# Kernel optimization log

Hardware: AMD Instinct MI355X
Metric: run time of the kernel (lower is better)

Reference implementation:

```python
import jax, jax.numpy as jnp
import numpy as np
from jax import lax


def setup_inputs() -> dict:
    key = jax.random.key(0)
    k1, k2, k3, k4 = jax.random.split(key, 4)
    H = 2048
    L = 3
    hidden_states = jax.random.normal(k1, (2, 4096, H), dtype=jnp.float32)
    Win = jax.random.normal(k2, (3 * H, H), dtype=jnp.float32) * (H ** -0.5)
    conv_w = jax.random.normal(k3, (H, 1, L), dtype=jnp.float32) * (L ** -0.5)
    Wout = jax.random.normal(k4, (H, H), dtype=jnp.float32) * (H ** -0.5)
    return {"hidden_states": hidden_states, "Win": Win, "conv_w": conv_w, "Wout": Wout}


def reference(hidden_states, Win, conv_w, Wout):
    H = hidden_states.shape[-1]
    L = conv_w.shape[-1]
    BCx = jnp.einsum('bsh,oh->bso', hidden_states, Win)  # (b, s, 3H)
    B, C, x = jnp.split(BCx, 3, axis=-1)
    Bx = jnp.transpose(B * x, (0, 2, 1))  # (b, H, s)
    # depthwise causal conv: left-pad L-1 so output length == s (torch pads both
    # sides then slices [..., :seqlen]; left-only padding is equivalent)
    conv_out = lax.conv_general_dilated(
        Bx, conv_w, window_strides=(1,), padding=[(L - 1, 0)],
        feature_group_count=H, dimension_numbers=('NCH', 'OIH', 'NCH'))
    y = C * jnp.transpose(conv_out, (0, 2, 1))  # (b, s, H)
    return jnp.einsum('bsh,oh->bso', y, Wout)
```

## Files before the change

### kernel.cpp

```cpp
#include <hip/hip_runtime.h>
#include <hip/hip_bf16.h>

typedef unsigned short u16;
typedef __attribute__((ext_vector_type(8))) short bf16x8;
typedef __attribute__((ext_vector_type(16))) float f32x16;

static __device__ __forceinline__ u16 f2bf(float f) {
    unsigned u = __float_as_uint(f);
    unsigned r = (u + 0x7fffu + ((u >> 16) & 1u)) >> 16;
    return (u16)r;
}
static __device__ __forceinline__ float bf2f(u16 u) {
    return __uint_as_float(((unsigned)u) << 16);
}

static __device__ __forceinline__ void async_copy16(const void* gptr, void* lptr) {
    __builtin_amdgcn_global_load_lds(
        (const __attribute__((address_space(1))) void*)gptr,
        (__attribute__((address_space(3))) void*)lptr, 16, 0, 0);
}

__global__ __launch_bounds__(256)
void cvt_all(const float* __restrict__ a, const float* __restrict__ b,
             const float* __restrict__ c,
             u16* __restrict__ oa, u16* __restrict__ ob, u16* __restrict__ oc) {
    int blk = blockIdx.x;
    const float* src; u16* dst; long base;
    if (blk < 16384)      { src = a; dst = oa; base = blk; }
    else if (blk < 28672) { src = b; dst = ob; base = blk - 16384; }
    else                  { src = c; dst = oc; base = blk - 28672; }
    long i = (base * 256 + threadIdx.x) * 4;
    float4 f = *(const float4*)(src + i);
    u16 o[4] = { f2bf(f.x), f2bf(f.y), f2bf(f.z), f2bf(f.w) };
    *(uint2*)(dst + i) = *(const uint2*)o;
}

template<bool BF16_OUT>
__global__ __launch_bounds__(256, 2)
void gemm_bt(const u16* __restrict__ A, const u16* __restrict__ B,
             void* __restrict__ Cout, int M, int N, int K) {
    __shared__ __align__(16) u16 As[256 * 32];
    __shared__ __align__(16) u16 Bs[128 * 32];

    const int t    = threadIdx.x;
    const int wave = t >> 6;
    const int lane = t & 63;
    const int wm   = (wave >> 1) * 128;
    const int wn   = (wave & 1) * 64;
    const int half = lane >> 5;
    const int l32  = lane & 31;

    const int id   = blockIdx.y * gridDim.x + blockIdx.x;
    const int cpx  = gridDim.x >> 3;
    const int xcd  = id & 7;
    const int loc  = id >> 3;
    const int bx   = xcd * cpx + (loc % cpx);
    const int by   = loc / cpx;

    const int rowA = by * 256;
    const int rowB = bx * 128;

    const int ar = t >> 2;
    const int ac = ((t & 3) ^ ((ar >> 1) & 3)) * 8;
    const u16* Ag[4]; const u16* Bg[2];
#pragma unroll
    for (int i = 0; i < 4; i++) Ag[i] = A + (long)(rowA + i * 64 + ar) * K + ac;
#pragma unroll
    for (int i = 0; i < 2; i++) Bg[i] = B + (long)(rowB + i * 64 + ar) * K + ac;
    u16* Asl[4]; u16* Bsl[2];
#pragma unroll
    for (int i = 0; i < 4; i++) Asl[i] = As + i * 2048 + t * 8;
#pragma unroll
    for (int i = 0; i < 2; i++) Bsl[i] = Bs + i * 2048 + t * 8;

    f32x16 acc[4][2] = {};

    for (int k0 = 0; k0 < K; k0 += 32) {
        __syncthreads();
#pragma unroll
        for (int i = 0; i < 4; i++) async_copy16(Ag[i] + k0, Asl[i]);
#pragma unroll
        for (int i = 0; i < 2; i++) async_copy16(Bg[i] + k0, Bsl[i]);
        __syncthreads();

        bf16x8 af[4][2], bg[2][2];
#pragma unroll
        for (int mi = 0; mi < 4; mi++)
#pragma unroll
            for (int ks = 0; ks < 2; ks++) {
                int row = wm + mi * 32 + l32;
                af[mi][ks] = *(const bf16x8*)(
                    As + row * 32 + (((ks * 2 + half) ^ ((row >> 1) & 3)) * 8));
            }
#pragma unroll
        for (int nj = 0; nj < 2; nj++)
#pragma unroll
            for (int ks = 0; ks < 2; ks++) {
                int row = wn + nj * 32 + l32;
                bg[nj][ks] = *(const bf16x8*)(
                    Bs + row * 32 + (((ks * 2 + half) ^ ((row >> 1) & 3)) * 8));
            }
#pragma unroll
        for (int ks = 0; ks < 2; ks++)
#pragma unroll
            for (int mi = 0; mi < 4; mi++)
#pragma unroll
                for (int nj = 0; nj < 2; nj++)
                    acc[mi][nj] = __builtin_amdgcn_mfma_f32_32x32x16_bf16(
                        af[mi][ks], bg[nj][ks], acc[mi][nj], 0, 0, 0);
    }

#pragma unroll
    for (int mi = 0; mi < 4; mi++) {
#pragma unroll
        for (int nj = 0; nj < 2; nj++) {
#pragma unroll
            for (int r = 0; r < 16; r++) {
                int rowt = (r & 3) + 8 * (r >> 2) + 4 * half;
                long m = rowA + wm + mi * 32 + rowt;
                long n = rowB + wn + nj * 32 + l32;
                float v = acc[mi][nj][r];
                if (BF16_OUT) ((u16*)Cout)[m * N + n] = f2bf(v);
                else          ((float*)Cout)[m * N + n] = v;
            }
        }
    }
}

union U16x8 { uint4 v; u16 u[8]; };

__global__ __launch_bounds__(256)
void conv_fuse(const u16* __restrict__ BCx, const float* __restrict__ cw,
               u16* __restrict__ y) {
    const int row = blockIdx.x;
    const int h0  = threadIdx.x * 8;
    const int sl  = row & 4095;
    const u16* r0 = BCx + (long)row * 6144;

    U16x8 B0, X0, C0, B1, X1, B2, X2;
    B0.v = *(const uint4*)(r0 + h0);
    C0.v = *(const uint4*)(r0 + 2048 + h0);
    X0.v = *(const uint4*)(r0 + 4096 + h0);
    if (sl >= 1) {
        B1.v = *(const uint4*)(r0 - 6144 + h0);
        X1.v = *(const uint4*)(r0 - 6144 + 4096 + h0);
    } else { B1.v = make_uint4(0,0,0,0); X1.v = make_uint4(0,0,0,0); }
    if (sl >= 2) {
        B2.v = *(const uint4*)(r0 - 12288 + h0);
        X2.v = *(const uint4*)(r0 - 12288 + 4096 + h0);
    } else { B2.v = make_uint4(0,0,0,0); X2.v = make_uint4(0,0,0,0); }

    U16x8 o;
#pragma unroll
    for (int i = 0; i < 8; i++) {
        int h = h0 + i;
        float bx0 = bf2f(B0.u[i]) * bf2f(X0.u[i]);
        float bx1 = bf2f(B1.u[i]) * bf2f(X1.u[i]);
        float bx2 = bf2f(B2.u[i]) * bf2f(X2.u[i]);
        float v = cw[h*3+2] * bx0 + cw[h*3+1] * bx1 + cw[h*3] * bx2;
        o.u[i] = f2bf(v * bf2f(C0.u[i]));
    }
    *(uint4*)(y + (long)row * 2048 + h0) = o.v;
}

extern "C" void kernel_launch(void* const* d_in, const int* in_sizes, int n_in,
                              void* d_out, int out_size, void* d_ws, size_t ws_size,
                              hipStream_t stream) {
    const float* hs   = (const float*)d_in[0];
    const float* Win  = (const float*)d_in[1];
    const float* cw   = (const float*)d_in[2];
    const float* Wout = (const float*)d_in[3];
    float* out = (float*)d_out;

    char* ws = (char*)d_ws;
    u16* hsb   = (u16*)(ws);
    u16* Winb  = (u16*)(ws +  33554432);
    u16* Woutb = (u16*)(ws +  58720256);
    u16* bcx   = (u16*)(ws +  67108864);
    u16* yb    = (u16*)(ws + 167772160);

    cvt_all<<<32768, 256, 0, stream>>>(hs, Win, Wout, hsb, Winb, Woutb);

    gemm_bt<true ><<<dim3(48, 32), 256, 0, stream>>>(hsb, Winb, bcx, 8192, 6144, 2048);

    conv_fuse<<<8192, 256, 0, stream>>>(bcx, cw, yb);

    gemm_bt<false><<<dim3(16, 32), 256, 0, stream>>>(yb, Woutb, out, 8192, 2048, 2048);
}
```

Measured before the change: 504.5 us.

## Rewrite bf16 GEMM as 8-wave 256x256 tile with double-buffered LDS pipeline

Result: faster. 437.0 us (-13.4%).

```diff
diff --git a/kernel.cpp b/kernel.cpp
--- a/kernel.cpp
+++ b/kernel.cpp
@@ -3,7 +3,7 @@
 
 typedef unsigned short u16;
 typedef __attribute__((ext_vector_type(8))) short bf16x8;
-typedef __attribute__((ext_vector_type(16))) float f32x16;
+typedef __attribute__((ext_vector_type(4))) float f32x4;
 
 static __device__ __forceinline__ u16 f2bf(float f) {
     unsigned u = __float_as_uint(f);
@@ -36,92 +36,158 @@
 }
 
 template<bool BF16_OUT>
-__global__ __launch_bounds__(256, 2)
-void gemm_bt(const u16* __restrict__ A, const u16* __restrict__ B,
-             void* __restrict__ Cout, int M, int N, int K) {
-    __shared__ __align__(16) u16 As[256 * 32];
-    __shared__ __align__(16) u16 Bs[128 * 32];
+__global__ __launch_bounds__(512, 2)
+void gemm_bt8(const u16* __restrict__ A, const u16* __restrict__ B,
+              void* __restrict__ Cout, int M, int N, int K) {
+    __shared__ __align__(16) u16 lds[65536];
 
     const int t    = threadIdx.x;
-    const int wave = t >> 6;
     const int lane = t & 63;
-    const int wm   = (wave >> 1) * 128;
-    const int wn   = (wave & 1) * 64;
-    const int half = lane >> 5;
-    const int l32  = lane & 31;
+    const int wm   = (t >> 6) >> 2;
+    const int wn   = (t >> 6) & 3;
+    const int l15  = lane & 15;
+    const int hi   = lane >> 4;
+    const int l7   = lane & 7;
 
     const int id   = blockIdx.y * gridDim.x + blockIdx.x;
     const int cpx  = gridDim.x >> 3;
-    const int xcd  = id & 7;
-    const int loc  = id >> 3;
-    const int bx   = xcd * cpx + (loc % cpx);
-    const int by   = loc / cpx;
-
-    const int rowA = by * 256;
-    const int rowB = bx * 128;
-
-    const int ar = t >> 2;
-    const int ac = ((t & 3) ^ ((ar >> 1) & 3)) * 8;
-    const u16* Ag[4]; const u16* Bg[2];
-#pragma unroll
-    for (int i = 0; i < 4; i++) Ag[i] = A + (long)(rowA + i * 64 + ar) * K + ac;
-#pragma unroll
-    for (int i = 0; i < 2; i++) Bg[i] = B + (long)(rowB + i * 64 + ar) * K + ac;
-    u16* Asl[4]; u16* Bsl[2];
-#pragma unroll
-    for (int i = 0; i < 4; i++) Asl[i] = As + i * 2048 + t * 8;
-#pragma unroll
-    for (int i = 0; i < 2; i++) Bsl[i] = Bs + i * 2048 + t * 8;
-
-    f32x16 acc[4][2] = {};
-
-    for (int k0 = 0; k0 < K; k0 += 32) {
-        __syncthreads();
-#pragma unroll
-        for (int i = 0; i < 4; i++) async_copy16(Ag[i] + k0, Asl[i]);
-#pragma unroll
-        for (int i = 0; i < 2; i++) async_copy16(Bg[i] + k0, Bsl[i]);
-        __syncthreads();
-
-        bf16x8 af[4][2], bg[2][2];
-#pragma unroll
-        for (int mi = 0; mi < 4; mi++)
-#pragma unroll
-            for (int ks = 0; ks < 2; ks++) {
-                int row = wm + mi * 32 + l32;
-                af[mi][ks] = *(const bf16x8*)(
-                    As + row * 32 + (((ks * 2 + half) ^ ((row >> 1) & 3)) * 8));
-            }
-#pragma unroll
-        for (int nj = 0; nj < 2; nj++)
-#pragma unroll
-            for (int ks = 0; ks < 2; ks++) {
-                int row = wn + nj * 32 + l32;
-                bg[nj][ks] = *(const bf16x8*)(
-                    Bs + row * 32 + (((ks * 2 + half) ^ ((row >> 1) & 3)) * 8));
-            }
+    const int bx   = (id & 7) * cpx + ((id >> 3) % cpx);
+    const int by   = (id >> 3) / cpx;
+    const long rowA = (long)by * 256;
+    const long rowB = (long)bx * 256;
+
+    const int pl0 = t >> 3;
+    const int slotcol = ((t & 7) ^ (pl0 & 7)) * 8;
+    const u16* Asrc[2][2]; const u16* Bsrc[2][2];
+#pragma unroll
+    for (int h = 0; h < 2; h++) {
+        int gA0 = h * 64 + pl0;
+        int gA1 = 128 + h * 64 + pl0;
+        Asrc[h][0] = A + (rowA + gA0) * K + slotcol;
+        Asrc[h][1] = A + (rowA + gA1) * K + slotcol;
+        int nB0 = (pl0 >> 5) * 64 + h * 32 + (pl0 & 31);
+        int nB1 = ((64 + pl0) >> 5) * 64 + h * 32 + (pl0 & 31);
+        Bsrc[h][0] = B + (rowB + nB0) * K + slotcol;
+        Bsrc[h][1] = B + (rowB + nB1) * K + slotcol;
+    }
+    const int t8 = t * 8;
+
+    auto STAGE = [&](int bufo, bool isB, int h, int kk) {
+        const u16* s0 = (isB ? Bsrc : Asrc)[h][0] + kk;
+        const u16* s1 = (isB ? Bsrc : Asrc)[h][1] + kk;
+        u16* d = lds + bufo + (isB ? 16384 : 0) + h * 8192 + t8;
+        async_copy16(s0, d);
+        async_copy16(s1, d + 4096);
+    };
+
+    const int aBase = wm * 4096 + l15 * 64;
+    const int bBase = 16384 + wn * 2048 + l15 * 64;
+    const int sOff0 = (hi ^ l7) * 8;
+    const int sOff1 = ((4 + hi) ^ l7) * 8;
+
+    bf16x8 af[4][2], bg0[2][2], bg1[2][2];
+    f32x4 acc[8][4] = {};
+
+    auto LOAD_AF = [&](int bufo, int Mq) {
+#pragma unroll
+        for (int m = 0; m < 4; m++) {
+            const u16* p = lds + bufo + Mq * 8192 + aBase + m * 1024;
+            af[m][0] = *(const bf16x8*)(p + sOff0);
+            af[m][1] = *(const bf16x8*)(p + sOff1);
+        }
+    };
+    auto LOAD_BG = [&](int bufo, int Nq, bf16x8 (*bg)[2]) {
+#pragma unroll
+        for (int n = 0; n < 2; n++) {
+            const u16* p = lds + bufo + Nq * 8192 + bBase + n * 1024;
+            bg[n][0] = *(const bf16x8*)(p + sOff0);
+            bg[n][1] = *(const bf16x8*)(p + sOff1);
+        }
+    };
+    auto MFMA_Q = [&](int Mq, int Nq, bf16x8 (*bg)[2]) {
+        __builtin_amdgcn_s_setprio(1);
 #pragma unroll
         for (int ks = 0; ks < 2; ks++)
 #pragma unroll
-            for (int mi = 0; mi < 4; mi++)
-#pragma unroll
-                for (int nj = 0; nj < 2; nj++)
-                    acc[mi][nj] = __builtin_amdgcn_mfma_f32_32x32x16_bf16(
-                        af[mi][ks], bg[nj][ks], acc[mi][nj], 0, 0, 0);
-    }
-
-#pragma unroll
-    for (int mi = 0; mi < 4; mi++) {
-#pragma unroll
-        for (int nj = 0; nj < 2; nj++) {
-#pragma unroll
-            for (int r = 0; r < 16; r++) {
-                int rowt = (r & 3) + 8 * (r >> 2) + 4 * half;
-                long m = rowA + wm + mi * 32 + rowt;
-                long n = rowB + wn + nj * 32 + l32;
+            for (int m = 0; m < 4; m++)
+#pragma unroll
+                for (int n = 0; n < 2; n++)
+                    acc[Mq * 4 + m][Nq * 2 + n] =
+                        __builtin_amdgcn_mfma_f32_16x16x32_bf16(
+                            af[m][ks], bg[n][ks], acc[Mq * 4 + m][Nq * 2 + n],
+                            0, 0, 0);
+        __builtin_amdgcn_s_setprio(0);
+    };
+
+#define BAR()   __builtin_amdgcn_s_barrier()
+#define WAITL() do { asm volatile("s_waitcnt lgkmcnt(0)" ::: "memory"); \
+                     __builtin_amdgcn_sched_barrier(0); } while (0)
+#define VM6()   asm volatile("s_waitcnt vmcnt(6)" ::: "memory")
+
+    STAGE(0, false, 0, 0);  STAGE(0, false, 1, 0);
+    STAGE(0, true,  0, 0);  STAGE(0, true,  1, 0);
+    STAGE(32768, false, 0, 64);
+    STAGE(32768, true,  0, 64);  STAGE(32768, true, 1, 64);
+    VM6();
+    BAR();
+
+#pragma unroll 1
+    for (int k0 = 0; k0 < K; k0 += 128) {
+        int kN1 = k0 + 64;
+        int kN2 = k0 + 128; if (kN2 >= K) kN2 = 0;
+        int kN3 = k0 + 192; if (kN3 >= K) kN3 -= K;
+        LOAD_AF(0, 0); LOAD_BG(0, 0, bg0);
+        STAGE(32768, false, 1, kN1);
+        BAR(); WAITL();
+        MFMA_Q(0, 0, bg0); BAR();
+        LOAD_BG(0, 1, bg1);
+        STAGE(0, false, 0, kN2);
+        BAR(); WAITL();
+        MFMA_Q(0, 1, bg1); BAR();
+        LOAD_AF(0, 1);
+        STAGE(0, true, 0, kN2);
+        BAR(); WAITL();
+        MFMA_Q(1, 0, bg0); BAR();
+        STAGE(0, true, 1, kN2);
+        VM6();
+        BAR();
+        MFMA_Q(1, 1, bg1); BAR();
+        LOAD_AF(32768, 0); LOAD_BG(32768, 0, bg0);
+        STAGE(0, false, 1, kN2);
+        BAR(); WAITL();
+        MFMA_Q(0, 0, bg0); BAR();
+        LOAD_BG(32768, 1, bg1);
+        STAGE(32768, false, 0, kN3);
+        BAR(); WAITL();
+        MFMA_Q(0, 1, bg1); BAR();
+        LOAD_AF(32768, 1);
+        STAGE(32768, true, 0, kN3);
+        BAR(); WAITL();
+        MFMA_Q(1, 0, bg0); BAR();
+        STAGE(32768, true, 1, kN3);
+        VM6();
+        BAR();
+        MFMA_Q(1, 1, bg1); BAR();
+    }
+    asm volatile("s_waitcnt vmcnt(0)" ::: "memory");
+
+#undef BAR
+#undef WAITL
+#undef VM6
+
+    const long crowBase = rowA + wm * 128 + hi * 4;
+    const long ccolBase = rowB + wn * 64 + l15;
+#pragma unroll
+    for (int mi = 0; mi < 8; mi++) {
+#pragma unroll
+        for (int nj = 0; nj < 4; nj++) {
+            long base = (crowBase + mi * 16) * N + ccolBase + nj * 16;
+#pragma unroll
+            for (int r = 0; r < 4; r++) {
                 float v = acc[mi][nj][r];
-                if (BF16_OUT) ((u16*)Cout)[m * N + n] = f2bf(v);
-                else          ((float*)Cout)[m * N + n] = v;
+                long idx = base + (long)r * N;
+                if (BF16_OUT) ((u16*)Cout)[idx] = f2bf(v);
+                else          ((float*)Cout)[idx] = v;
             }
         }
     }
@@ -181,9 +247,9 @@
 
     cvt_all<<<32768, 256, 0, stream>>>(hs, Win, Wout, hsb, Winb, Woutb);
 
-    gemm_bt<true ><<<dim3(48, 32), 256, 0, stream>>>(hsb, Winb, bcx, 8192, 6144, 2048);
+    gemm_bt8<true ><<<dim3(24, 32), 512, 0, stream>>>(hsb, Winb, bcx, 8192, 6144, 2048);
 
     conv_fuse<<<8192, 256, 0, stream>>>(bcx, cw, yb);
 
-    gemm_bt<false><<<dim3(16, 32), 256, 0, stream>>>(yb, Woutb, out, 8192, 2048, 2048);
-}
+    gemm_bt8<false><<<dim3(8, 32), 512, 0, stream>>>(yb, Woutb, out, 8192, 2048, 2048);
+}
```

## Rewrite GEMM as 256x256 tile, 8-wave kernel with 4-stage async LDS pipeline

Applied to the files above, without the earlier changes.

Result: faster. 467.3 us (-7.4%).

```diff
diff --git a/kernel.cpp b/kernel.cpp
--- a/kernel.cpp
+++ b/kernel.cpp
@@ -36,79 +36,94 @@
 }
 
 template<bool BF16_OUT>
-__global__ __launch_bounds__(256, 2)
-void gemm_bt(const u16* __restrict__ A, const u16* __restrict__ B,
-             void* __restrict__ Cout, int M, int N, int K) {
-    __shared__ __align__(16) u16 As[256 * 32];
-    __shared__ __align__(16) u16 Bs[128 * 32];
+__global__ __launch_bounds__(512, 2)
+void gemm_bt8(const u16* __restrict__ A, const u16* __restrict__ B,
+              void* __restrict__ Cout, int M, int N, int K) {
+    __shared__ __align__(16) u16 lds[65536];
 
     const int t    = threadIdx.x;
-    const int wave = t >> 6;
     const int lane = t & 63;
-    const int wm   = (wave >> 1) * 128;
-    const int wn   = (wave & 1) * 64;
-    const int half = lane >> 5;
+    const int wm   = (t >> 6) >> 2;
+    const int wn   = (t >> 6) & 3;
     const int l32  = lane & 31;
+    const int hi   = lane >> 5;
 
     const int id   = blockIdx.y * gridDim.x + blockIdx.x;
     const int cpx  = gridDim.x >> 3;
-    const int xcd  = id & 7;
-    const int loc  = id >> 3;
-    const int bx   = xcd * cpx + (loc % cpx);
-    const int by   = loc / cpx;
-
-    const int rowA = by * 256;
-    const int rowB = bx * 128;
-
-    const int ar = t >> 2;
-    const int ac = ((t & 3) ^ ((ar >> 1) & 3)) * 8;
-    const u16* Ag[4]; const u16* Bg[2];
-#pragma unroll
-    for (int i = 0; i < 4; i++) Ag[i] = A + (long)(rowA + i * 64 + ar) * K + ac;
-#pragma unroll
-    for (int i = 0; i < 2; i++) Bg[i] = B + (long)(rowB + i * 64 + ar) * K + ac;
-    u16* Asl[4]; u16* Bsl[2];
-#pragma unroll
-    for (int i = 0; i < 4; i++) Asl[i] = As + i * 2048 + t * 8;
-#pragma unroll
-    for (int i = 0; i < 2; i++) Bsl[i] = Bs + i * 2048 + t * 8;
-
+    const int bx   = (id & 7) * cpx + ((id >> 3) % cpx);
+    const int by   = (id >> 3) / cpx;
+    const long rowA = (long)by * 256;
+    const long rowB = (long)bx * 256;
+
+    const int sr  = t >> 2;
+    const int kcs = ((t & 3) ^ ((sr >> 1) & 3)) * 8;
+    const u16* Asrc0 = A + (rowA + sr) * (long)K + kcs;
+    const u16* Asrc1 = Asrc0 + 128 * (long)K;
+    const u16* Bsrc0 = B + (rowB + sr) * (long)K + kcs;
+    const u16* Bsrc1 = Bsrc0 + 128 * (long)K;
+    u16* const dA = lds + t * 8;
+    u16* const dB = lds + 8192 + t * 8;
+
+    const int sw = (l32 >> 1) & 3;
+    const int c0 = (hi ^ sw) * 8;
+    const int c1 = ((2 + hi) ^ sw) * 8;
+    const int aO = (wm * 128 + l32) * 32;
+    const int bO = 8192 + (wn * 64 + l32) * 32;
+
+    bf16x8 afA[4], bgA[2], afB[4], bgB[2];
     f32x16 acc[4][2] = {};
 
-    for (int k0 = 0; k0 < K; k0 += 32) {
-        __syncthreads();
-#pragma unroll
-        for (int i = 0; i < 4; i++) async_copy16(Ag[i] + k0, Asl[i]);
-#pragma unroll
-        for (int i = 0; i < 2; i++) async_copy16(Bg[i] + k0, Bsl[i]);
-        __syncthreads();
-
-        bf16x8 af[4][2], bg[2][2];
-#pragma unroll
-        for (int mi = 0; mi < 4; mi++)
-#pragma unroll
-            for (int ks = 0; ks < 2; ks++) {
-                int row = wm + mi * 32 + l32;
-                af[mi][ks] = *(const bf16x8*)(
-                    As + row * 32 + (((ks * 2 + half) ^ ((row >> 1) & 3)) * 8));
-            }
-#pragma unroll
-        for (int nj = 0; nj < 2; nj++)
-#pragma unroll
-            for (int ks = 0; ks < 2; ks++) {
-                int row = wn + nj * 32 + l32;
-                bg[nj][ks] = *(const bf16x8*)(
-                    Bs + row * 32 + (((ks * 2 + half) ^ ((row >> 1) & 3)) * 8));
-            }
-#pragma unroll
-        for (int ks = 0; ks < 2; ks++)
-#pragma unroll
-            for (int mi = 0; mi < 4; mi++)
-#pragma unroll
-                for (int nj = 0; nj < 2; nj++)
-                    acc[mi][nj] = __builtin_amdgcn_mfma_f32_32x32x16_bf16(
-                        af[mi][ks], bg[nj][ks], acc[mi][nj], 0, 0, 0);
+    auto STAGE_A = [&](int bufo, int kk) {
+        async_copy16(Asrc0 + kk, dA + bufo);
+        async_copy16(Asrc1 + kk, dA + bufo + 4096);
+    };
+    auto STAGE_B = [&](int bufo, int kk) {
+        async_copy16(Bsrc0 + kk, dB + bufo);
+        async_copy16(Bsrc1 + kk, dB + bufo + 4096);
+    };
+    auto LOADS = [&](int bufo, int cOff, bf16x8* af, bf16x8* bg) {
+#pragma unroll
+        for (int m = 0; m < 4; m++)
+            af[m] = *(const bf16x8*)(lds + bufo + aO + m * 1024 + cOff);
+#pragma unroll
+        for (int n = 0; n < 2; n++)
+            bg[n] = *(const bf16x8*)(lds + bufo + bO + n * 1024 + cOff);
+    };
+    auto MF = [&](bf16x8* af, bf16x8* bg) {
+        __builtin_amdgcn_s_setprio(1);
+#pragma unroll
+        for (int m = 0; m < 4; m++)
+#pragma unroll
+            for (int n = 0; n < 2; n++)
+                acc[m][n] = __builtin_amdgcn_mfma_f32_32x32x16_bf16(
+                    af[m], bg[n], acc[m][n], 0, 0, 0);
+        __builtin_amdgcn_s_setprio(0);
+    };
+
+    STAGE_A(0, 0);          STAGE_B(0, 0);
+    STAGE_A(16384, 32);     STAGE_B(16384, 32);
+    STAGE_A(32768, 64);     STAGE_B(32768, 64);
+    asm volatile("s_waitcnt vmcnt(4)" ::: "memory");
+    __builtin_amdgcn_s_barrier();
+    LOADS(0, c0, afA, bgA);
+
+    const int NT = K >> 5;
+#pragma unroll 4
+    for (int i = 0; i < NT; i++) {
+        const int bufR = (i & 3) << 14;
+        const int bufN = ((i + 1) & 3) << 14;
+        const int bufS = ((i + 3) & 3) << 14;
+        int kk = (i + 3) << 5; if (kk >= K) kk = 0;
+        LOADS(bufR, c1, afB, bgB);
+        STAGE_A(bufS, kk);
+        MF(afA, bgA);
+        LOADS(bufN, c0, afA, bgA);
+        STAGE_B(bufS, kk);
+        MF(afB, bgB);
+        asm volatile("s_waitcnt vmcnt(4)" ::: "memory");
+        __builtin_amdgcn_s_barrier();
     }
+    asm volatile("s_waitcnt vmcnt(0)" ::: "memory");
 
 #pragma unroll
     for (int mi = 0; mi < 4; mi++) {
@@ -116,9 +131,9 @@
         for (int nj = 0; nj < 2; nj++) {
 #pragma unroll
             for (int r = 0; r < 16; r++) {
-                int rowt = (r & 3) + 8 * (r >> 2) + 4 * half;
-                long m = rowA + wm + mi * 32 + rowt;
-                long n = rowB + wn + nj * 32 + l32;
+                int rowt = (r & 3) + 8 * (r >> 2) + 4 * hi;
+                long m = rowA + wm * 128 + mi * 32 + rowt;
+                long n = rowB + wn * 64 + nj * 32 + l32;
                 float v = acc[mi][nj][r];
                 if (BF16_OUT) ((u16*)Cout)[m * N + n] = f2bf(v);
                 else          ((float*)Cout)[m * N + n] = v;
@@ -181,9 +196,9 @@
 
     cvt_all<<<32768, 256, 0, stream>>>(hs, Win, Wout, hsb, Winb, Woutb);
 
-    gemm_bt<true ><<<dim3(48, 32), 256, 0, stream>>>(hsb, Winb, bcx, 8192, 6144, 2048);
+    gemm_bt8<true ><<<dim3(24, 32), 512, 0, stream>>>(hsb, Winb, bcx, 8192, 6144, 2048);
 
     conv_fuse<<<8192, 256, 0, stream>>>(bcx, cw, yb);
 
-    gemm_bt<false><<<dim3(16, 32), 256, 0, stream>>>(yb, Woutb, out, 8192, 2048, 2048);
-}
+    gemm_bt8<false><<<dim3(8, 32), 512, 0, stream>>>(yb, Woutb, out, 8192, 2048, 2048);
+}
```
